# Optimization experiments

Measured on AMD Instinct MI355X. Metric: run time of the kernel, lower is better.

The kernel has to match this reference:

```python
import jax, jax.numpy as jnp
import numpy as np
from jax import lax

EPS = 1e-5

def _silu(x):
    return x * jax.nn.sigmoid(x)

def _mamba_seq(x, ln_w, ln_b, in_w, conv_w, conv_b, xp_w, dt_w, dt_b, A_log, Dp, out_w):
    # x: [B, L, dim] token sequence
    di = conv_w.shape[0]          # d_inner
    ds = A_log.shape[1]           # d_state
    dtr = dt_w.shape[1]           # dt_rank
    kw = conv_w.shape[2]          # d_conv
    # LayerNorm
    mu = jnp.mean(x, axis=-1, keepdims=True)
    var = jnp.mean((x - mu) ** 2, axis=-1, keepdims=True)
    xn = (x - mu) * lax.rsqrt(var + EPS) * ln_w + ln_b
    # in_proj -> (x, z)
    xz = xn @ in_w.T                       # [B,L,2*di]
    xs, z = xz[..., :di], xz[..., di:]
    # causal depthwise conv1d over L
    xc = lax.conv_general_dilated(xs.transpose(0, 2, 1), conv_w, (1,),
                                  [(kw - 1, 0)], feature_group_count=di,
                                  dimension_numbers=('NCH', 'OIH', 'NCH'))
    xc = _silu(xc + conv_b[None, :, None]).transpose(0, 2, 1)   # [B,L,di]
    # x_proj -> dt, B, C
    dbc = xc @ xp_w.T                      # [B,L,dtr+2*ds]
    dt = jax.nn.softplus(dbc[..., :dtr] @ dt_w.T + dt_b)        # [B,L,di]
    Bm = dbc[..., dtr:dtr + ds]            # [B,L,ds]
    Cm = dbc[..., dtr + ds:]               # [B,L,ds]
    A = -jnp.exp(A_log)                    # [di,ds]
    dA = jnp.exp(dt[..., None] * A)        # [B,L,di,ds]
    dBu = (dt * xc)[..., None] * Bm[:, :, None, :]              # [B,L,di,ds]
    # selective scan: h_t = dA_t * h_{t-1} + dBu_t (parallel associative scan)
    def comb(e1, e2):
        a1, b1 = e1
        a2, b2 = e2
        return a1 * a2, a2 * b1 + b2
    _, h = lax.associative_scan(comb, (dA, dBu), axis=1)
    y = jnp.einsum('blds,bls->bld', h, Cm) + xc * Dp
    return (y * _silu(z)) @ out_w.T

def _mamba_block(x5, *p):
    # x5: [B,C,D,H,W] -> flatten spatial dims to tokens
    B, C = x5.shape[:2]
    xf = x5.reshape(B, C, -1).transpose(0, 2, 1)   # [B,L,C]
    y = _mamba_seq(xf, *p)
    return y.transpose(0, 2, 1).reshape(x5.shape)

def _conv3d(x, w, b):
    return lax.conv_general_dilated(x, w, (1, 1, 1), [(1, 1)] * 3,
                                    dimension_numbers=('NCDHW', 'OIDHW', 'NCDHW')) \
           + b[None, :, None, None, None]

def _bn3d(x, g, b):
    # BatchNorm3d in training mode: batch statistics over (B,D,H,W)
    m = jnp.mean(x, axis=(0, 2, 3, 4), keepdims=True)
    v = jnp.mean((x - m) ** 2, axis=(0, 2, 3, 4), keepdims=True)
    return (x - m) * lax.rsqrt(v + EPS) * g.reshape(1, -1, 1, 1, 1) + b.reshape(1, -1, 1, 1, 1)

def _mamba_params(key, dim, d_state=16, d_conv=4, expand=2):
    di = expand * dim
    dtr = max(1, -(-dim // 16))
    ks = jax.random.split(key, 5)
    return {
        'ln_w': jnp.ones((dim,), jnp.float32),
        'ln_b': jnp.zeros((dim,), jnp.float32),
        'in_w': jax.random.normal(ks[0], (2 * di, dim), jnp.float32) * (dim ** -0.5),
        'conv_w': jax.random.normal(ks[1], (di, 1, d_conv), jnp.float32) * 0.3,
        'conv_b': jnp.zeros((di,), jnp.float32),
        'xp_w': jax.random.normal(ks[2], (dtr + 2 * d_state, di), jnp.float32) * (di ** -0.5),
        'dt_w': jax.random.normal(ks[3], (di, dtr), jnp.float32) * (dtr ** -0.5),
        'dt_b': jnp.log(jnp.expm1(jnp.full((di,), 0.01, jnp.float32))),
        'A_log': jnp.log(jnp.tile(jnp.arange(1, d_state + 1, dtype=jnp.float32)[None, :], (di, 1))),
        'D': jnp.ones((di,), jnp.float32),
        'out_w': jax.random.normal(ks[4], (dim, di), jnp.float32) * (di ** -0.5),
    }

def setup_inputs() -> dict:
    key = jax.random.key(0)
    k = jax.random.split(key, 8)
    inp = {
        'l': jax.random.normal(k[0], (1, 16, 16, 48, 48), jnp.float32),
        's': jax.random.normal(k[1], (1, 16, 16, 48, 48), jnp.float32),
    }
    for name, p in _mamba_params(k[2], 32).items():
        inp['m1_' + name] = p
    for name, p in _mamba_params(k[3], 16).items():
        inp['m2_' + name] = p
    inp['c1_w'] = jax.random.normal(k[4], (16, 32, 3, 3, 3), jnp.float32) * ((32 * 27) ** -0.5)
    inp['c1_b'] = jnp.zeros((16,), jnp.float32)
    inp['bn1_g'] = jnp.ones((16,), jnp.float32)
    inp['bn1_b'] = jnp.zeros((16,), jnp.float32)
    inp['c2_w'] = jax.random.normal(k[5], (16, 16, 3, 3, 3), jnp.float32) * ((16 * 27) ** -0.5)
    inp['c2_b'] = jnp.zeros((16,), jnp.float32)
    inp['bn2_g'] = jnp.ones((16,), jnp.float32)
    inp['bn2_b'] = jnp.zeros((16,), jnp.float32)
    return inp

def reference(l, s,
              m1_ln_w, m1_ln_b, m1_in_w, m1_conv_w, m1_conv_b, m1_xp_w, m1_dt_w, m1_dt_b, m1_A_log, m1_D, m1_out_w,
              m2_ln_w, m2_ln_b, m2_in_w, m2_conv_w, m2_conv_b, m2_xp_w, m2_dt_w, m2_dt_b, m2_A_log, m2_D, m2_out_w,
              c1_w, c1_b, bn1_g, bn1_b, c2_w, c2_b, bn2_g, bn2_b):
    x = jnp.concatenate([l, s], axis=1)                         # [B,32,D,H,W]
    x = _mamba_block(x, m1_ln_w, m1_ln_b, m1_in_w, m1_conv_w, m1_conv_b,
                     m1_xp_w, m1_dt_w, m1_dt_b, m1_A_log, m1_D, m1_out_w) + x
    x = _bn3d(_conv3d(x, c1_w, c1_b), bn1_g, bn1_b)             # [B,16,D,H,W]
    x = _mamba_block(x, m2_ln_w, m2_ln_b, m2_in_w, m2_conv_w, m2_conv_b,
                     m2_xp_w, m2_dt_w, m2_dt_b, m2_A_log, m2_D, m2_out_w) + x
    x = _bn3d(_conv3d(x, c2_w, c2_b), bn2_g, bn2_b)
    return x
```

## Files before the change

kernel.cpp:

```cpp
#include <hip/hip_runtime.h>
#include <math.h>

#define L_TOT 36864
#define BN_EPS 1e-5f
#define PCH 45000

typedef __attribute__((ext_vector_type(8))) short bf16x8;
typedef __attribute__((ext_vector_type(4))) float f32x4;

__device__ __forceinline__ float fsigmoid(float x){ return 1.f/(1.f+__expf(-x)); }
__device__ __forceinline__ float fsoftplus(float x){
  float e = __expf(x);
  return (x>20.f)? x : __logf(1.f+e);
}
__device__ __forceinline__ unsigned short f2bf(float x){
  union { float f; unsigned u; } cv; cv.f = x;
  unsigned r = (cv.u + 0x7FFFu + ((cv.u>>16)&1u)) >> 16;
  return (unsigned short)r;
}
__host__ __device__ constexpr int off3c(int r){
  return (r>=27) ? 0 : ((r/9)-1)*2500 + (((r%9)/3)-1)*50 + ((r%3)-1);
}

template<int DIM, int DI, int DTR, bool DOBN, bool SETUP>
__global__ __launch_bounds__(256) void k_front(
    const float* __restrict__ x0, const float* __restrict__ x1,
    const float* __restrict__ bstats, const float* __restrict__ bg, const float* __restrict__ bbp,
    const float* __restrict__ lnw, const float* __restrict__ lnb,
    const float* __restrict__ inw,
    const float* __restrict__ cw, const float* __restrict__ cb,
    const float* __restrict__ xpw,
    const float* __restrict__ dtw, const float* __restrict__ dtb,
    const float* __restrict__ Alog,
    float* __restrict__ xcg, float* __restrict__ zg,
    float* __restrict__ dtpg, float* __restrict__ Bg, float* __restrict__ Cg,
    float* __restrict__ aggA, float* __restrict__ aggB,
    const float* __restrict__ cvw1, unsigned short* __restrict__ wA1,
    const float* __restrict__ cvw2, unsigned short* __restrict__ wA2,
    float* __restrict__ stats, float* __restrict__ bfz)
{
  constexpr int TCH  = 48;
  constexpr int ROWS = DTR + 32;
  constexpr int NSH  = 256/DI;
  constexpr int SPB  = 16/NSH;
  constexpr int CH   = DI*16;
  constexpr int NRT  = (2*DI)/16;
  constexpr int R0SZ = DI*64;
  constexpr int O_SXC = R0SZ;
  constexpr int O_SB  = O_SXC + DI*49;
  constexpr int O_SC  = O_SB + 16*49;
  constexpr int O_DTP = O_SC + 16*49;
  constexpr int O_WA  = O_DTP + DTR*48;
  constexpr int SMEM  = O_WA + NRT*256 + 16;
  __shared__ float sm[SMEM];

  const int tid   = threadIdx.x;
  const int chunk = blockIdx.x;
  const int t0    = chunk*TCH;

  if constexpr (SETUP){
    for (int idx = blockIdx.x*256 + tid; idx < 16*PCH; idx += 768*256)
      bfz[idx] = 0.f;
    const int b = blockIdx.x;
    if (b < 4){
      int k = b*256 + tid;
      if (k < 864){
        int ic = k & 31, r = k >> 5;
        for (int m=0;m<16;m++){
          float v = (r < 27) ? cvw1[m*32*27 + ic*27 + r] : 0.f;
          wA1[(((k>>3)*16) + m)*8 + (k&7)] = f2bf(v);
        }
      }
    } else if (b < 6){
      int k = (b-4)*256 + tid;
      if (k < 448){
        int ic = k & 15, r = k >> 4;
        for (int m=0;m<16;m++){
          float v = (r < 27) ? cvw2[m*16*27 + ic*27 + r] : 0.f;
          wA2[(((k>>3)*16) + m)*8 + (k&7)] = f2bf(v);
        }
      }
    } else if (b == 6){
      if (tid < 64) stats[tid] = 0.f;
    }
  }

  const int i   = tid & 63;
  const int r0w = __builtin_amdgcn_readfirstlane(tid >> 6);

  {
    unsigned short* winAl = (unsigned short*)&sm[O_WA];
    unsigned short* xnl   = (unsigned short*)&sm[O_SXC];
    for (int sidx = tid; sidx < NRT*64; sidx += 256){
      int ln  = sidx & 63;
      int row = (sidx >> 6)*16 + (ln & 15);
      int k0  = (ln >> 4)*8;
      unsigned short* wp = winAl + sidx*8;
#pragma unroll
      for (int j = 0; j < 8; j++){
        int k = k0 + j;
        wp[j] = (k < DIM) ? f2bf(inw[row*DIM + k]) : (unsigned short)0;
      }
    }
    float xn[DIM];
    const int t = t0 - 3 + i;
    const bool valid = (i < 51 && t >= 0);
#pragma unroll
    for (int c = 0; c < DIM; c++){
      float v = 0.f;
      if (valid){
        if constexpr (DOBN){
          float raw = x0[c*L_TOT + t];
          float bm = bstats[2*c]*(1.f/L_TOT);
          float bv = bstats[2*c+1]*(1.f/L_TOT) - bm*bm;
          v = (raw - bm)*rsqrtf(bv+BN_EPS)*bg[c] + bbp[c];
        } else {
          v = (c < 16) ? x0[c*L_TOT + t] : x1[(c-16)*L_TOT + t];
        }
      }
      xn[c] = v;
    }
    float s = 0.f, s2 = 0.f;
#pragma unroll
    for (int c = 0; c < DIM; c++){ s += xn[c]; s2 += xn[c]*xn[c]; }
    float m  = s*(1.f/DIM);
    float var = s2*(1.f/DIM) - m*m;
    float rs = rsqrtf(var + BN_EPS);
    unsigned short* xr = xnl + i*32;
#pragma unroll
    for (int c = 0; c < DIM; c++) xr[c] = f2bf((xn[c]-m)*rs*lnw[c] + lnb[c]);
    if constexpr (DIM < 32){
#pragma unroll
      for (int c = DIM; c < 32; c++) xr[c] = 0;
    }
  }
  __syncthreads();

  {
    const unsigned short* winAl = (const unsigned short*)&sm[O_WA];
    const unsigned short* xnl   = (const unsigned short*)&sm[O_SXC];
    const int ln  = tid & 63;
    const int wv  = tid >> 6;
    const int col = wv*16 + (ln & 15);
    bf16x8 bfr = *reinterpret_cast<const bf16x8*>(xnl + (size_t)col*32 + (ln>>4)*8);
    f32x4 zero = {0.f,0.f,0.f,0.f};
#pragma unroll
    for (int rt = 0; rt < NRT; rt++){
      bf16x8 af = *reinterpret_cast<const bf16x8*>(winAl + (size_t)(rt*64 + ln)*8);
      f32x4 dd = __builtin_amdgcn_mfma_f32_16x16x32_bf16(af, bfr, zero, 0, 0, 0);
#pragma unroll
      for (int r = 0; r < 4; r++){
        int row = rt*16 + (ln>>4)*4 + r;
        if (row < DI){
          if (col < 51) sm[row*64 + col] = (t0 == 0 && col < 3) ? 0.f : dd[r];
        } else {
          if (col >= 3 && col < 51) zg[(row-DI)*L_TOT + t0 + col - 3] = dd[r];
        }
      }
    }
  }
  __syncthreads();

  for (int idx = tid; idx < DI*48; idx += 256){
    int d = idx / 48, j = idx - d*48;
    const float* xr = &sm[d*64 + j];
    float acc = cb[d] + cw[d*4+0]*xr[0] + cw[d*4+1]*xr[1]
                      + cw[d*4+2]*xr[2] + cw[d*4+3]*xr[3];
    sm[O_SXC + d*49 + j] = acc * fsigmoid(acc);
  }
  __syncthreads();

  {
    constexpr int NR = (ROWS + 3) / 4;
    float acc[NR];
#pragma unroll
    for (int rr = 0; rr < NR; rr++) acc[rr] = 0.f;
    for (int db = 0; db < DI; db += 16){
      float xcol[16];
#pragma unroll
      for (int k = 0; k < 16; k++) xcol[k] = sm[O_SXC + (db+k)*49 + i];
#pragma unroll
      for (int rr = 0; rr < NR; rr++){
        int r = r0w + rr*4;
        if (r < ROWS){
          float a2 = 0.f;
#pragma unroll
          for (int k = 0; k < 16; k++) a2 += xcol[k]*xpw[r*DI + db + k];
          acc[rr] += a2;
        }
      }
    }
    if (i < 48){
#pragma unroll
      for (int rr = 0; rr < NR; rr++){
        int r = r0w + rr*4;
        if (r < ROWS){
          if (r < DTR)          sm[O_DTP + r*48 + i] = acc[rr];
          else if (r < DTR+16)  sm[O_SB + (r-DTR)*49 + i] = acc[rr];
          else                  sm[O_SC + (r-DTR-16)*49 + i] = acc[rr];
        }
      }
    }
  }
  __syncthreads();

  for (int idx = tid; idx < DI*48; idx += 256){
    int d = idx / 48, j = idx - d*48;
    float pre = dtb[d] + dtw[d*DTR]*sm[O_DTP + j];
    if (DTR > 1) pre += dtw[d*DTR + DTR-1]*sm[O_DTP + (DTR-1)*48 + j];
    sm[d*49 + j] = fsoftplus(pre);
  }
  __syncthreads();

  for (int idx = tid; idx < DI*12; idx += 256){
    int d = idx / 12, q = idx - d*12;
    float4 v = make_float4(sm[O_SXC + d*49 + q*4+0], sm[O_SXC + d*49 + q*4+1],
                           sm[O_SXC + d*49 + q*4+2], sm[O_SXC + d*49 + q*4+3]);
    *reinterpret_cast<float4*>(xcg + d*L_TOT + t0 + q*4) = v;
  }
  for (int idx = tid; idx < ROWS*12; idx += 256){
    int r = idx / 12, q = idx - r*12;
    const float* src; float* dst;
    if (r < DTR)        { src = &sm[O_DTP + r*48 + q*4];          dst = dtpg + r*L_TOT + t0 + q*4; }
    else if (r < DTR+16){ src = &sm[O_SB + (r-DTR)*49 + q*4];     dst = Bg + (r-DTR)*L_TOT + t0 + q*4; }
    else                { src = &sm[O_SC + (r-DTR-16)*49 + q*4];  dst = Cg + (r-DTR-16)*L_TOT + t0 + q*4; }
    *reinterpret_cast<float4*>(dst) = make_float4(src[0], src[1], src[2], src[3]);
  }

  {
    const int d  = tid / NSH;
    const int sh = tid - d*NSH;
    float Av[SPB], Ar[SPB], Br[SPB];
#pragma unroll
    for (int j = 0; j < SPB; j++){
      Av[j] = -__expf(Alog[d*16 + sh*SPB + j]);
      Ar[j] = 1.f; Br[j] = 0.f;
    }
    for (int t = 0; t < TCH; t++){
      float dtv = sm[d*49 + t];
      float bb2 = dtv * sm[O_SXC + d*49 + t];
#pragma unroll
      for (int j = 0; j < SPB; j++){
        float a2 = __expf(dtv*Av[j]);
        Ar[j] *= a2;
        Br[j] = a2*Br[j] + bb2*sm[O_SB + (sh*SPB+j)*49 + t];
      }
    }
    const int o = chunk*CH + tid*SPB;
    if constexpr (SPB == 4){
      *reinterpret_cast<float4*>(&aggA[o]) = make_float4(Ar[0],Ar[1],Ar[2],Ar[3]);
      *reinterpret_cast<float4*>(&aggB[o]) = make_float4(Br[0],Br[1],Br[2],Br[3]);
    } else {
      *reinterpret_cast<float2*>(&aggA[o]) = make_float2(Ar[0],Ar[1]);
      *reinterpret_cast<float2*>(&aggB[o]) = make_float2(Br[0],Br[1]);
    }
  }
}

template<int NCH>
__global__ __launch_bounds__(256) void k_carry(const float* __restrict__ aggA,
                        const float* __restrict__ aggB,
                        float* __restrict__ carry, int CH) {
  constexpr int SEG = NCH/16;
  const int chl = threadIdx.x & 15;
  const int seg = threadIdx.x >> 4;
  const int ch  = blockIdx.x*16 + chl;
  const int c0  = seg*SEG;
  float a = 1.f, b = 0.f;
  for (int cb=c0; cb<c0+SEG; cb+=8){
    float av[8], bv[8];
#pragma unroll
    for (int k=0;k<8;k++){ av[k]=aggA[(cb+k)*CH+ch]; bv[k]=aggB[(cb+k)*CH+ch]; }
#pragma unroll
    for (int k=0;k<8;k++){ a = a*av[k]; b = av[k]*b + bv[k]; }
  }
  __shared__ float sa[16][17], sb[16][17];
  sa[seg][chl]=a; sb[seg][chl]=b;
  __syncthreads();
  if (threadIdx.x < 16){
    float pa=1.f, pb=0.f;
    for (int g=0; g<16; g++){
      float ca=sa[g][threadIdx.x], cb2=sb[g][threadIdx.x];
      sa[g][threadIdx.x]=pa; sb[g][threadIdx.x]=pb;
      float na = pa*ca;
      float nb = ca*pb + cb2;
      pa=na; pb=nb;
    }
  }
  __syncthreads();
  float h = sb[seg][chl];
  for (int cb=c0; cb<c0+SEG; cb+=8){
    float av[8], bv[8];
#pragma unroll
    for (int k=0;k<8;k++){ av[k]=aggA[(cb+k)*CH+ch]; bv[k]=aggB[(cb+k)*CH+ch]; }
#pragma unroll
    for (int k=0;k<8;k++){ carry[(cb+k)*CH+ch]=h; h = av[k]*h + bv[k]; }
  }
}

template<int DIM, int DI, int DTR, int RES>
__global__ __launch_bounds__(256) void k_back(
    const float* __restrict__ xcg, const float* __restrict__ zg,
    const float* __restrict__ dtpg, const float* __restrict__ Bg, const float* __restrict__ Cg,
    const float* __restrict__ dtw, const float* __restrict__ dtb,
    const float* __restrict__ Alog, const float* __restrict__ Dp,
    const float* __restrict__ carry,
    const float* __restrict__ ow,
    const float* __restrict__ r0src, const float* __restrict__ r1src,
    const float* __restrict__ bstats, const float* __restrict__ bg, const float* __restrict__ bbp,
    unsigned short* __restrict__ rp)
{
  constexpr int TCH = 48;
  constexpr int NSH = 256/DI;
  constexpr int SPB = 16/NSH;
  constexpr int ROWS = DTR + 32;
  constexpr int O_SXC = 0;
  constexpr int O_SDT = O_SXC + DI*49;
  constexpr int O_SB  = O_SDT + DI*49;
  constexpr int O_SC  = O_SB + 16*49;
  constexpr int O_SY  = O_SC + 16*49;
  constexpr int O_DTP = O_SY + DI*49;
  constexpr int SMEM  = O_DTP + DTR*48 + 64;
  __shared__ float sm[SMEM];
  const int tid   = threadIdx.x;
  const int chunk = blockIdx.x;
  const int t0    = chunk*TCH;

  for (int idx = tid; idx < DI*12; idx += 256){
    int d = idx / 12, q = idx - d*12;
    float4 v = *reinterpret_cast<const float4*>(xcg + d*L_TOT + t0 + q*4);
    sm[O_SXC + d*49 + q*4+0] = v.x; sm[O_SXC + d*49 + q*4+1] = v.y;
    sm[O_SXC + d*49 + q*4+2] = v.z; sm[O_SXC + d*49 + q*4+3] = v.w;
  }
  for (int idx = tid; idx < ROWS*12; idx += 256){
    int r = idx / 12, q = idx - r*12;
    const float* src; float* dst;
    if (r < DTR)        { src = dtpg + r*L_TOT + t0 + q*4;         dst = &sm[O_DTP + r*48 + q*4]; }
    else if (r < DTR+16){ src = Bg + (r-DTR)*L_TOT + t0 + q*4;     dst = &sm[O_SB + (r-DTR)*49 + q*4]; }
    else                { src = Cg + (r-DTR-16)*L_TOT + t0 + q*4;  dst = &sm[O_SC + (r-DTR-16)*49 + q*4]; }
    float4 v = *reinterpret_cast<const float4*>(src);
    dst[0] = v.x; dst[1] = v.y; dst[2] = v.z; dst[3] = v.w;
  }
  __syncthreads();
  for (int idx = tid; idx < DI*48; idx += 256){
    int d = idx / 48, j = idx - d*48;
    float pre = dtb[d] + dtw[d*DTR]*sm[O_DTP + j];
    if (DTR > 1) pre += dtw[d*DTR + DTR-1]*sm[O_DTP + 48 + j];
    sm[O_SDT + d*49 + j] = fsoftplus(pre);
  }
  __syncthreads();

  {
    const int d  = tid / NSH;
    const int sh = tid - d*NSH;
    float Av[SPB], h[SPB];
#pragma unroll
    for (int j = 0; j < SPB; j++){
      Av[j] = -__expf(Alog[d*16 + sh*SPB + j]);
      h[j]  = carry[chunk*(DI*16) + tid*SPB + j];
    }
    const float Dv = Dp[d];
    for (int t = 0; t < TCH; t++){
      float dtv = sm[O_SDT + d*49 + t];
      float xcv = sm[O_SXC + d*49 + t];
      float bb2 = dtv*xcv;
      float p = 0.f;
#pragma unroll
      for (int j = 0; j < SPB; j++){
        float a2 = __expf(dtv*Av[j]);
        h[j] = a2*h[j] + bb2*sm[O_SB + (sh*SPB+j)*49 + t];
        p += h[j]*sm[O_SC + (sh*SPB+j)*49 + t];
      }
#pragma unroll
      for (int o = 1; o < NSH; o <<= 1) p += __shfl_xor(p, o);
      if (sh == 0) sm[O_SY + d*49 + t] = p + xcv*Dv;
    }
  }
  __syncthreads();
  for (int idx = tid; idx < DI*12; idx += 256){
    int d = idx / 12, q = idx - d*12;
    float4 zv = *reinterpret_cast<const float4*>(zg + d*L_TOT + t0 + q*4);
    sm[O_SY + d*49 + q*4+0] *= zv.x*fsigmoid(zv.x);
    sm[O_SY + d*49 + q*4+1] *= zv.y*fsigmoid(zv.y);
    sm[O_SY + d*49 + q*4+2] *= zv.z*fsigmoid(zv.z);
    sm[O_SY + d*49 + q*4+3] *= zv.w*fsigmoid(zv.w);
  }
  __syncthreads();

  {
    const int col = tid & 63;
    const int r0w = __builtin_amdgcn_readfirstlane(tid >> 6);
    constexpr int NO = DIM/4;
    float acc[NO];
#pragma unroll
    for (int rr = 0; rr < NO; rr++) acc[rr] = 0.f;
    for (int db = 0; db < DI; db += 16){
      float ycol[16];
#pragma unroll
      for (int k = 0; k < 16; k++) ycol[k] = sm[O_SY + (db+k)*49 + col];
#pragma unroll
      for (int rr = 0; rr < NO; rr++){
        int r = r0w + rr*4;
        float a2 = 0.f;
#pragma unroll
        for (int k = 0; k < 16; k++) a2 += ycol[k]*ow[r*DI + db + k];
        acc[rr] += a2;
      }
    }
    if (col < 48){
      const int t  = t0 + col;
      const int zz = chunk / 48, yy = chunk - zz*48;
      const int pb = (zz+1)*2500 + (yy+1)*50 + (col+1);
#pragma unroll
      for (int rr = 0; rr < NO; rr++){
        int r = r0w + rr*4;
        float res;
        if (RES == 0){
          res = (r < 16) ? r0src[r*L_TOT + t] : r1src[(r-16)*L_TOT + t];
        } else {
          float bm = bstats[2*r]*(1.f/L_TOT);
          float bv = bstats[2*r+1]*(1.f/L_TOT) - bm*bm;
          res = (r0src[r*L_TOT + t] - bm)*rsqrtf(bv+BN_EPS)*bg[r] + bbp[r];
        }
        rp[r*PCH + pb] = f2bf(acc[rr] + res);
      }
    }
  }
}

template<int IC>
__global__ __launch_bounds__(256) void k_conv_mfma(const unsigned short* __restrict__ bin,
                         const unsigned short* __restrict__ wA,
                         const float* __restrict__ bias, float* __restrict__ out,
                         float* __restrict__ stats) {
  constexpr int NKB = (IC==32) ? 27 : 14;
  __shared__ float sred[32];
  if (threadIdx.x < 32) sred[threadIdx.x] = 0.f;
  __syncthreads();
  const int lane = threadIdx.x & 63;
  const int n = lane & 15, quad = lane >> 4;
  const int tile = blockIdx.x*4 + (threadIdx.x >> 6);
  const int t = tile*16 + n;
  int zz = t / 2304;
  int r2 = t - zz*2304;
  int yy = r2 / 48;
  int xx = r2 - yy*48;
  int pb = (zz+1)*2500 + (yy+1)*50 + (xx+1);
  const unsigned short* bp[8];
#pragma unroll
  for (int j=0;j<8;j++){
    int e = quad*8 + j;
    int ic = (IC==32) ? e : (e & 15);
    bp[j] = bin + ic*PCH + pb;
  }
  const int rq = (IC==32) ? 0 : (quad >> 1);
  f32x4 acc = {0.f, 0.f, 0.f, 0.f};
#pragma unroll
  for (int kb=0; kb<NKB; kb++){
    bf16x8 af = *reinterpret_cast<const bf16x8*>(wA + (size_t)((kb*4+quad)*16 + n)*8);
    int off;
    if (IC==32) off = off3c(kb);
    else        off = rq ? off3c(2*kb+1) : off3c(2*kb);
    bf16x8 bf;
#pragma unroll
    for (int j=0;j<8;j++) bf[j] = (short)bp[j][off];
    acc = __builtin_amdgcn_mfma_f32_16x16x32_bf16(af, bf, acc, 0, 0, 0);
  }
  float vs[4];
#pragma unroll
  for (int reg=0; reg<4; reg++){
    int m = quad*4 + reg;
    float v = acc[reg] + bias[m];
    out[m*L_TOT + t] = v;
    vs[reg] = v;
  }
#pragma unroll
  for (int reg=0; reg<4; reg++){
    float a = vs[reg], b2 = vs[reg]*vs[reg];
#pragma unroll
    for (int o=1; o<16; o<<=1){ a += __shfl_xor(a,o); b2 += __shfl_xor(b2,o); }
    if (n == 0){
      atomicAdd(&sred[quad*4+reg], a);
      atomicAdd(&sred[16 + quad*4+reg], b2);
    }
  }
  __syncthreads();
  if (threadIdx.x < 16){
    atomicAdd(&stats[2*threadIdx.x],   sred[threadIdx.x]);
    atomicAdd(&stats[2*threadIdx.x+1], sred[16+threadIdx.x]);
  }
}

__global__ void k_bn_norm4(const float* __restrict__ raw, const float* __restrict__ stats,
                           const float* __restrict__ g, const float* __restrict__ b,
                           float* __restrict__ out) {
  int i = blockIdx.x*256 + threadIdx.x;
  int c = i / (L_TOT/4);
  int tq = i - c*(L_TOT/4);
  float m = stats[2*c]*(1.f/L_TOT);
  float v = stats[2*c+1]*(1.f/L_TOT) - m*m;
  float sc = rsqrtf(v+BN_EPS)*g[c];
  float bs = b[c] - m*sc;
  float4 x = *reinterpret_cast<const float4*>(raw + c*L_TOT + tq*4);
  float4 o = make_float4(x.x*sc+bs, x.y*sc+bs, x.z*sc+bs, x.w*sc+bs);
  *reinterpret_cast<float4*>(out + c*L_TOT + tq*4) = o;
}

extern "C" void kernel_launch(void* const* d_in, const int* in_sizes, int n_in,
                              void* d_out, int out_size, void* d_ws, size_t ws_size,
                              hipStream_t stream) {
  const float* l        = (const float*)d_in[0];
  const float* s        = (const float*)d_in[1];
  const float* m1_ln_w  = (const float*)d_in[2];
  const float* m1_ln_b  = (const float*)d_in[3];
  const float* m1_in_w  = (const float*)d_in[4];
  const float* m1_cw    = (const float*)d_in[5];
  const float* m1_cb    = (const float*)d_in[6];
  const float* m1_xp_w  = (const float*)d_in[7];
  const float* m1_dt_w  = (const float*)d_in[8];
  const float* m1_dt_b  = (const float*)d_in[9];
  const float* m1_Alog  = (const float*)d_in[10];
  const float* m1_D     = (const float*)d_in[11];
  const float* m1_out_w = (const float*)d_in[12];
  const float* m2_ln_w  = (const float*)d_in[13];
  const float* m2_ln_b  = (const float*)d_in[14];
  const float* m2_in_w  = (const float*)d_in[15];
  const float* m2_cw    = (const float*)d_in[16];
  const float* m2_cb    = (const float*)d_in[17];
  const float* m2_xp_w  = (const float*)d_in[18];
  const float* m2_dt_w  = (const float*)d_in[19];
  const float* m2_dt_b  = (const float*)d_in[20];
  const float* m2_Alog  = (const float*)d_in[21];
  const float* m2_D     = (const float*)d_in[22];
  const float* m2_out_w = (const float*)d_in[23];
  const float* c1_w     = (const float*)d_in[24];
  const float* c1_b     = (const float*)d_in[25];
  const float* bn1_g    = (const float*)d_in[26];
  const float* bn1_b    = (const float*)d_in[27];
  const float* c2_w     = (const float*)d_in[28];
  const float* c2_b     = (const float*)d_in[29];
  const float* bn2_g    = (const float*)d_in[30];
  const float* bn2_b    = (const float*)d_in[31];

  float* ws = (float*)d_ws;
  const size_t L = L_TOT;
  float* xc1      = ws;
  float* z1       = ws + 64*L;
  float* B1       = ws + 128*L;
  float* C1       = ws + 144*L;
  float* dtp1     = ws + 160*L;
  float* conv1raw = ws + 162*L;
  float* xc2      = ws + 178*L;
  float* z2       = ws + 210*L;
  float* conv2raw = ws + 242*L;
  float* aggA     = ws + 258*L;
  float* aggB     = aggA + 786432;
  float* carry    = aggB + 786432;
  float* stats1   = ws + 322*L;
  float* stats2   = stats1 + 32;
  unsigned short* bfin = (unsigned short*)(ws + 323*L);
  unsigned short* wA1  = (unsigned short*)(ws + 343*L);
  unsigned short* wA2  = wA1 + 13824;

  k_front<32,64,2,false,true><<<768,256,0,stream>>>(l, s, stats1, bn1_g, bn1_b,
      m1_ln_w, m1_ln_b, m1_in_w, m1_cw, m1_cb, m1_xp_w, m1_dt_w, m1_dt_b, m1_Alog,
      xc1, z1, dtp1, B1, C1, aggA, aggB,
      c1_w, wA1, c2_w, wA2, stats1, (float*)bfin);
  k_carry<768><<<64,256,0,stream>>>(aggA, aggB, carry, 1024);
  k_back<32,64,2,0><<<768,256,0,stream>>>(xc1, z1, dtp1, B1, C1,
      m1_dt_w, m1_dt_b, m1_Alog, m1_D, carry, m1_out_w, l, s,
      stats1, bn1_g, bn1_b, bfin);
  k_conv_mfma<32><<<576,256,0,stream>>>(bfin, wA1, c1_b, conv1raw, stats1);

  k_front<16,32,1,true,false><<<768,256,0,stream>>>(conv1raw, conv1raw, stats1, bn1_g, bn1_b,
      m2_ln_w, m2_ln_b, m2_in_w, m2_cw, m2_cb, m2_xp_w, m2_dt_w, m2_dt_b, m2_Alog,
      xc2, z2, dtp1, B1, C1, aggA, aggB,
      nullptr, nullptr, nullptr, nullptr, nullptr, nullptr);
  k_carry<768><<<32,256,0,stream>>>(aggA, aggB, carry, 512);
  k_back<16,32,1,1><<<768,256,0,stream>>>(xc2, z2, dtp1, B1, C1,
      m2_dt_w, m2_dt_b, m2_Alog, m2_D, carry, m2_out_w, conv1raw, conv1raw,
      stats1, bn1_g, bn1_b, bfin);
  k_conv_mfma<16><<<576,256,0,stream>>>(bfin, wA2, c2_b, conv2raw, stats2);
  k_bn_norm4<<<576,256,0,stream>>>(conv2raw, stats2, bn2_g, bn2_b, (float*)d_out);
}
```

Before: 283.1 us.

## Use bf16 MFMA for x_proj and out_proj matmuls in Mamba kernels

Replaces the scalar FP32 inner-product loops for the x_proj (dt/B/C) and out_proj matmuls with bf16 16x16x32 MFMA instructions. Each block converts weights into MFMA fragment layout in shared memory and stores activations transposed as bf16, then distributes 16x16 output tiles across waves. This aims to cut the scalar FMA and repeated global weight-load cost, at the price of bf16 rounding of activations and weights, extra shared memory, and per-block weight conversion overhead.

```diff
diff --git a/kernel.cpp b/kernel.cpp
--- a/kernel.cpp
+++ b/kernel.cpp
@@ -45,13 +45,17 @@
   constexpr int SPB  = 16/NSH;
   constexpr int CH   = DI*16;
   constexpr int NRT  = (2*DI)/16;
+  constexpr int NKC  = DI/32;
+  constexpr int NRX  = 3;
   constexpr int R0SZ = DI*64;
   constexpr int O_SXC = R0SZ;
   constexpr int O_SB  = O_SXC + DI*49;
   constexpr int O_SC  = O_SB + 16*49;
   constexpr int O_DTP = O_SC + 16*49;
   constexpr int O_WA  = O_DTP + DTR*48;
-  constexpr int SMEM  = O_WA + NRT*256 + 16;
+  constexpr int OWASZ = ((NRT > NRX*NKC) ? NRT : NRX*NKC)*256;
+  constexpr int O_XCP = O_WA + OWASZ;
+  constexpr int SMEM  = O_XCP + 24*DI + 16;
   __shared__ float sm[SMEM];
 
   const int tid   = threadIdx.x;
@@ -161,44 +165,53 @@
   }
   __syncthreads();
 
-  for (int idx = tid; idx < DI*48; idx += 256){
-    int d = idx / 48, j = idx - d*48;
-    const float* xr = &sm[d*64 + j];
-    float acc = cb[d] + cw[d*4+0]*xr[0] + cw[d*4+1]*xr[1]
-                      + cw[d*4+2]*xr[2] + cw[d*4+3]*xr[3];
-    sm[O_SXC + d*49 + j] = acc * fsigmoid(acc);
-  }
-  __syncthreads();
-
-  {
-    constexpr int NR = (ROWS + 3) / 4;
-    float acc[NR];
-#pragma unroll
-    for (int rr = 0; rr < NR; rr++) acc[rr] = 0.f;
-    for (int db = 0; db < DI; db += 16){
-      float xcol[16];
-#pragma unroll
-      for (int k = 0; k < 16; k++) xcol[k] = sm[O_SXC + (db+k)*49 + i];
-#pragma unroll
-      for (int rr = 0; rr < NR; rr++){
-        int r = r0w + rr*4;
-        if (r < ROWS){
-          float a2 = 0.f;
-#pragma unroll
-          for (int k = 0; k < 16; k++) a2 += xcol[k]*xpw[r*DI + db + k];
-          acc[rr] += a2;
-        }
-      }
-    }
-    if (i < 48){
-#pragma unroll
-      for (int rr = 0; rr < NR; rr++){
-        int r = r0w + rr*4;
-        if (r < ROWS){
-          if (r < DTR)          sm[O_DTP + r*48 + i] = acc[rr];
-          else if (r < DTR+16)  sm[O_SB + (r-DTR)*49 + i] = acc[rr];
-          else                  sm[O_SC + (r-DTR-16)*49 + i] = acc[rr];
-        }
+  {
+    unsigned short* xcp = (unsigned short*)&sm[O_XCP];
+    for (int idx = tid; idx < DI*48; idx += 256){
+      int d = idx / 48, j = idx - d*48;
+      const float* xr = &sm[d*64 + j];
+      float acc = cb[d] + cw[d*4+0]*xr[0] + cw[d*4+1]*xr[1]
+                        + cw[d*4+2]*xr[2] + cw[d*4+3]*xr[3];
+      float v = acc * fsigmoid(acc);
+      sm[O_SXC + d*49 + j] = v;
+      xcp[j*DI + d] = f2bf(v);
+    }
+    unsigned short* wfr = (unsigned short*)&sm[O_WA];
+    for (int sidx = tid; sidx < NRX*NKC*64; sidx += 256){
+      int ln = sidx & 63;
+      int fi = sidx >> 6;
+      int rt = fi / NKC, kc = fi - rt*NKC;
+      int row = rt*16 + (ln & 15);
+      int k0  = kc*32 + (ln>>4)*8;
+      unsigned short* wp = wfr + sidx*8;
+#pragma unroll
+      for (int j = 0; j < 8; j++)
+        wp[j] = (row < ROWS) ? f2bf(xpw[row*DI + k0 + j]) : (unsigned short)0;
+    }
+  }
+  __syncthreads();
+
+  {
+    const unsigned short* wfr = (const unsigned short*)&sm[O_WA];
+    const unsigned short* xcp = (const unsigned short*)&sm[O_XCP];
+    const int ln = tid & 63;
+    const int wv = tid >> 6;
+    for (int job = wv; job < NRX*3; job += 4){
+      int rt = job / 3, ct = job - rt*3;
+      int col = ct*16 + (ln & 15);
+      f32x4 acc = {0.f,0.f,0.f,0.f};
+#pragma unroll
+      for (int kc = 0; kc < NKC; kc++){
+        bf16x8 af  = *reinterpret_cast<const bf16x8*>(wfr + (size_t)((rt*NKC+kc)*64 + ln)*8);
+        bf16x8 bfr = *reinterpret_cast<const bf16x8*>(xcp + (size_t)col*DI + kc*32 + (ln>>4)*8);
+        acc = __builtin_amdgcn_mfma_f32_16x16x32_bf16(af, bfr, acc, 0, 0, 0);
+      }
+#pragma unroll
+      for (int r = 0; r < 4; r++){
+        int row = rt*16 + (ln>>4)*4 + r;
+        if (row < DTR)           sm[O_DTP + row*48 + col] = acc[r];
+        else if (row < DTR+16)   sm[O_SB + (row-DTR)*49 + col] = acc[r];
+        else if (row < ROWS)     sm[O_SC + (row-DTR-16)*49 + col] = acc[r];
       }
     }
   }
@@ -314,6 +327,8 @@
   constexpr int NSH = 256/DI;
   constexpr int SPB = 16/NSH;
   constexpr int ROWS = DTR + 32;
+  constexpr int NRO = DIM/16;
+  constexpr int NKC = DI/32;
   constexpr int O_SXC = 0;
   constexpr int O_SDT = O_SXC + DI*49;
   constexpr int O_SB  = O_SDT + DI*49;
@@ -377,52 +392,65 @@
     }
   }
   __syncthreads();
-  for (int idx = tid; idx < DI*12; idx += 256){
-    int d = idx / 12, q = idx - d*12;
-    float4 zv = *reinterpret_cast<const float4*>(zg + d*L_TOT + t0 + q*4);
-    sm[O_SY + d*49 + q*4+0] *= zv.x*fsigmoid(zv.x);
-    sm[O_SY + d*49 + q*4+1] *= zv.y*fsigmoid(zv.y);
-    sm[O_SY + d*49 + q*4+2] *= zv.z*fsigmoid(zv.z);
-    sm[O_SY + d*49 + q*4+3] *= zv.w*fsigmoid(zv.w);
-  }
-  __syncthreads();
-
-  {
-    const int col = tid & 63;
-    const int r0w = __builtin_amdgcn_readfirstlane(tid >> 6);
-    constexpr int NO = DIM/4;
-    float acc[NO];
-#pragma unroll
-    for (int rr = 0; rr < NO; rr++) acc[rr] = 0.f;
-    for (int db = 0; db < DI; db += 16){
-      float ycol[16];
-#pragma unroll
-      for (int k = 0; k < 16; k++) ycol[k] = sm[O_SY + (db+k)*49 + col];
-#pragma unroll
-      for (int rr = 0; rr < NO; rr++){
-        int r = r0w + rr*4;
-        float a2 = 0.f;
-#pragma unroll
-        for (int k = 0; k < 16; k++) a2 += ycol[k]*ow[r*DI + db + k];
-        acc[rr] += a2;
-      }
-    }
-    if (col < 48){
+
+  {
+    unsigned short* yp  = (unsigned short*)&sm[O_SDT];
+    unsigned short* wfr = (unsigned short*)&sm[O_SXC];
+    for (int sidx = tid; sidx < NRO*NKC*64; sidx += 256){
+      int ln = sidx & 63;
+      int fi = sidx >> 6;
+      int rt = fi / NKC, kc = fi - rt*NKC;
+      int row = rt*16 + (ln & 15);
+      int k0  = kc*32 + (ln>>4)*8;
+      unsigned short* wp = wfr + sidx*8;
+#pragma unroll
+      for (int j = 0; j < 8; j++) wp[j] = f2bf(ow[row*DI + k0 + j]);
+    }
+    for (int idx = tid; idx < DI*12; idx += 256){
+      int d = idx / 12, q = idx - d*12;
+      float4 zv = *reinterpret_cast<const float4*>(zg + d*L_TOT + t0 + q*4);
+      float y0 = sm[O_SY + d*49 + q*4+0];
+      float y1 = sm[O_SY + d*49 + q*4+1];
+      float y2 = sm[O_SY + d*49 + q*4+2];
+      float y3 = sm[O_SY + d*49 + q*4+3];
+      yp[(q*4+0)*DI + d] = f2bf(y0 * zv.x*fsigmoid(zv.x));
+      yp[(q*4+1)*DI + d] = f2bf(y1 * zv.y*fsigmoid(zv.y));
+      yp[(q*4+2)*DI + d] = f2bf(y2 * zv.z*fsigmoid(zv.z));
+      yp[(q*4+3)*DI + d] = f2bf(y3 * zv.w*fsigmoid(zv.w));
+    }
+  }
+  __syncthreads();
+
+  {
+    const unsigned short* yp  = (const unsigned short*)&sm[O_SDT];
+    const unsigned short* wfr = (const unsigned short*)&sm[O_SXC];
+    const int ln = tid & 63;
+    const int wv = tid >> 6;
+    const int zz = chunk / 48, yy = chunk - zz*48;
+    for (int job = wv; job < NRO*3; job += 4){
+      int rt = job / 3, ct = job - rt*3;
+      int col = ct*16 + (ln & 15);
+      f32x4 acc = {0.f,0.f,0.f,0.f};
+#pragma unroll
+      for (int kc = 0; kc < NKC; kc++){
+        bf16x8 af  = *reinterpret_cast<const bf16x8*>(wfr + (size_t)((rt*NKC+kc)*64 + ln)*8);
+        bf16x8 bfr = *reinterpret_cast<const bf16x8*>(yp + (size_t)col*DI + kc*32 + (ln>>4)*8);
+        acc = __builtin_amdgcn_mfma_f32_16x16x32_bf16(af, bfr, acc, 0, 0, 0);
+      }
       const int t  = t0 + col;
-      const int zz = chunk / 48, yy = chunk - zz*48;
       const int pb = (zz+1)*2500 + (yy+1)*50 + (col+1);
 #pragma unroll
-      for (int rr = 0; rr < NO; rr++){
-        int r = r0w + rr*4;
+      for (int r = 0; r < 4; r++){
+        int row = rt*16 + (ln>>4)*4 + r;
         float res;
         if (RES == 0){
-          res = (r < 16) ? r0src[r*L_TOT + t] : r1src[(r-16)*L_TOT + t];
+          res = (row < 16) ? r0src[row*L_TOT + t] : r1src[(row-16)*L_TOT + t];
         } else {
-          float bm = bstats[2*r]*(1.f/L_TOT);
-          float bv = bstats[2*r+1]*(1.f/L_TOT) - bm*bm;
-          res = (r0src[r*L_TOT + t] - bm)*rsqrtf(bv+BN_EPS)*bg[r] + bbp[r];
+          float bm = bstats[2*row]*(1.f/L_TOT);
+          float bv = bstats[2*row+1]*(1.f/L_TOT) - bm*bm;
+          res = (r0src[row*L_TOT + t] - bm)*rsqrtf(bv+BN_EPS)*bg[row] + bbp[row];
         }
-        rp[r*PCH + pb] = f2bf(acc[rr] + res);
+        rp[row*PCH + pb] = f2bf(acc[r] + res);
       }
     }
   }
```

Measured after the change: 270.8 us. 4.3% less time.
